# Optimization experiments

Hardware: AMD Instinct MI355X
Metric: run time of the kernel (lower is better)

Reference implementation:

```python
import jax, jax.numpy as jnp
import numpy as np

# norse LICell parameters: tau_mem_inv given as 1/0.001; others at norse defaults
DT = 0.001          # LICell default dt (module's self.dt is never passed to the cell)
TAU_MEM_INV = 1000.0
TAU_SYN_INV = 200.0
V_LEAK = 0.0


def setup_inputs() -> dict:
    key = jax.random.key(0)
    k1, k2 = jax.random.split(key)
    x = jax.random.normal(k1, (256, 1, 512, 512), dtype=jnp.float32)   # [T, C=1, H, W]
    kernel = jax.random.normal(k2, (5, 5), dtype=jnp.float32)          # square conv kernel
    return {"x": x, "kernel": kernel}


def reference(x, kernel):
    T, C, H, W = x.shape

    # Leaky-integrator (norse li_feed_forward_step) over time:
    #   v' = v + dt*tau_mem_inv*((v_leak - v) + i)
    #   i' = i - dt*tau_syn_inv*i + x_t
    # output at each step is v'.
    def step(carry, xt):
        v, i = carry
        v_new = v + DT * TAU_MEM_INV * ((V_LEAK - v) + i)
        i_new = i - DT * TAU_SYN_INV * i + xt
        return (v_new, i_new), v_new

    zeros = jnp.zeros((C, H, W), x.dtype)
    _, vs = jax.lax.scan(step, (zeros, zeros), x)  # [T, C, H, W]

    # Per-timestep 1->1 channel conv with 'same' padding, batched over T at once.
    k = kernel.shape[0]
    pad = (k - 1) // 2
    w = kernel[None, None]  # [O=1, I=1, k, k]
    out = jax.lax.conv_general_dilated(
        vs, w, window_strides=(1, 1),
        padding=[(pad, pad), (pad, pad)],
        dimension_numbers=("NCHW", "OIHW", "NCHW"),
    )
    return out  # [T, 1, H, W]
```

## Files before the change

### kernel.cpp

```cpp
#include <hip/hip_runtime.h>

#define T_STEPS 256
#define IMG 512
#define HW (IMG * IMG)
#define TW 32
#define TH 8
#define HTW 40
#define HTH 12
#define NCHK 120
#define BUF_DW 512
#define NBUF 12

__device__ __align__(16) float g_zeropage[8] = {0, 0, 0, 0, 0, 0, 0, 0};

typedef const __attribute__((address_space(1))) unsigned int* gptr_t;
typedef __attribute__((address_space(3))) unsigned int* lptr_t;
typedef float vf4 __attribute__((ext_vector_type(4)));
typedef float vf2 __attribute__((ext_vector_type(2)));

__launch_bounds__(64)
__global__ void conv_li_kernel(const float* __restrict__ x,
                               const float* __restrict__ kern,
                               float* __restrict__ out) {
    __shared__ __align__(16) float lds[NBUF][BUF_DW];
    const int tid = threadIdx.x;
    const int bid = blockIdx.x;
    const int vbid = (bid & 7) * 128 + (bid >> 3);
    const int bx = vbid & 15;
    const int by = vbid >> 4;

    float kw[25];
#pragma unroll
    for (int i = 0; i < 25; ++i)
        kw[i] = __int_as_float(__builtin_amdgcn_readfirstlane(__float_as_int(kern[i])));

    const float* srcA; const float* srcB; bool okA, okB;
    {
        int c = tid;
        int row = c / 10, cc = c - row * 10;
        int gy = by * TH + row - 2, gx = bx * TW + cc * 4 - 4;
        okA = (gy >= 0) && (gy < IMG) && (gx >= 0) && (gx <= IMG - 4);
        srcA = x + (size_t)(okA ? gy : 0) * IMG + (okA ? gx : 0);
        c = tid + 64;
        row = c / 10; cc = c - row * 10;
        gy = by * TH + row - 2; gx = bx * TW + cc * 4 - 4;
        okB = (c < NCHK) && (gy >= 0) && (gy < IMG) && (gx >= 0) && (gx <= IMG - 4);
        srcB = x + (size_t)(okB ? gy : 0) * IMG + (okB ? gx : 0);
    }

    auto GLDS = [&](int bi, int tf) {
        const float* pA = okA ? srcA + (size_t)tf * HW : g_zeropage;
        const float* pB = okB ? srcB + (size_t)tf * HW : g_zeropage;
        __builtin_amdgcn_global_load_lds((gptr_t)pA, (lptr_t)&lds[bi][0], 16, 0, 0);
        __builtin_amdgcn_global_load_lds((gptr_t)pB, (lptr_t)&lds[bi][256], 16, 0, 0);
    };
    auto BATCH = [&](int bufbase, int f0) {
#pragma unroll
        for (int j = 0; j < 4; ++j) {
            int tf = f0 + j; if (tf > T_STEPS - 1) tf = T_STEPS - 1;
            GLDS(bufbase + j, tf);
        }
    };

    const int q = tid & 7;
    const int rr = tid >> 3;
    const size_t obase = (size_t)(by * TH + rr) * IMG + bx * TW + q * 4;

    vf2 stA = {0.f, 0.f}, stB = {0.f, 0.f};

    auto STEP = [&](int bi, int t) {
        vf2 A0 = {0.f, 0.f}, A1 = {0.f, 0.f}, A2 = {0.f, 0.f}, A3 = {0.f, 0.f};
        const float* Bp = &lds[bi][rr * HTW + q * 4];
#pragma unroll
        for (int dy = 0; dy < 5; ++dy) {
            const float* L = Bp + dy * HTW;
            vf4 c0 = *(const vf4*)(L);
            vf4 c1 = *(const vf4*)(L + 4);
            vf4 c2 = *(const vf4*)(L + 8);
            vf2 P0 = {c0.z, c0.w};
            vf2 P1 = {c1.x, c1.y};
            vf2 P2 = {c1.z, c1.w};
            vf2 P3 = {c2.x, c2.y};
            const float k0 = kw[dy * 5 + 0], k1 = kw[dy * 5 + 1], k2 = kw[dy * 5 + 2];
            const float k3 = kw[dy * 5 + 3], k4 = kw[dy * 5 + 4];
            const vf2 K01 = {k0, k1}, K23 = {k2, k3}, K40 = {k4, 0.f};
            const vf2 K0h = {0.f, k0}, K12 = {k1, k2}, K34 = {k3, k4};
            A0 = __builtin_elementwise_fma(K01, P0, A0);
            A0 = __builtin_elementwise_fma(K23, P1, A0);
            A0 = __builtin_elementwise_fma(K40, P2, A0);
            A1 = __builtin_elementwise_fma(K0h, P0, A1);
            A1 = __builtin_elementwise_fma(K12, P1, A1);
            A1 = __builtin_elementwise_fma(K34, P2, A1);
            A2 = __builtin_elementwise_fma(K01, P1, A2);
            A2 = __builtin_elementwise_fma(K23, P2, A2);
            A2 = __builtin_elementwise_fma(K40, P3, A2);
            A3 = __builtin_elementwise_fma(K0h, P1, A3);
            A3 = __builtin_elementwise_fma(K12, P2, A3);
            A3 = __builtin_elementwise_fma(K34, P3, A3);
        }
        vf4 s = {stA.x, stA.y, stB.x, stB.y};
        __builtin_nontemporal_store(s, (vf4*)(out + (size_t)t * HW + obase));
        vf2 accA = {A0.x + A0.y, A1.x + A1.y};
        vf2 accB = {A2.x + A2.y, A3.x + A3.y};
        const vf2 m02 = {-0.2f, -0.2f};
        stA = __builtin_elementwise_fma(m02, stA, stA) + accA;
        stB = __builtin_elementwise_fma(m02, stB, stB) + accB;
    };

    BATCH(0, 0);
    BATCH(4, 4);

    asm volatile("s_waitcnt vmcnt(8)" ::: "memory");
    STEP(0, 0); STEP(1, 1); STEP(2, 2); STEP(3, 3);
    BATCH(8, 8);

#pragma clang loop unroll(disable)
    for (int sg = 0; sg < 21; ++sg) {
        const int t0 = 4 + sg * 12;
        asm volatile("s_waitcnt vmcnt(12)" ::: "memory");
        STEP(4, t0 + 0); STEP(5, t0 + 1); STEP(6, t0 + 2); STEP(7, t0 + 3);
        BATCH(0, t0 + 8);
        asm volatile("s_waitcnt vmcnt(12)" ::: "memory");
        STEP(8, t0 + 4); STEP(9, t0 + 5); STEP(10, t0 + 6); STEP(11, t0 + 7);
        BATCH(4, t0 + 12);
        asm volatile("s_waitcnt vmcnt(12)" ::: "memory");
        STEP(0, t0 + 8); STEP(1, t0 + 9); STEP(2, t0 + 10); STEP(3, t0 + 11);
        BATCH(8, t0 + 16);
    }
}

extern "C" void kernel_launch(void* const* d_in, const int* in_sizes, int n_in,
                              void* d_out, int out_size, void* d_ws, size_t ws_size,
                              hipStream_t stream) {
    const float* x = (const float*)d_in[0];
    const float* kern = (const float*)d_in[1];
    float* out = (float*)d_out;

    conv_li_kernel<<<dim3(1024), dim3(64), 0, stream>>>(x, kern, out);
}
```

Measured before the change: 97.11 us.

## Shift output column mapping by two so LDS reads use two aligned vf4 loads

Each thread's output window moves right by two columns, so its 5x5 stencil inputs fit in two aligned vf4 LDS reads per row instead of three. Stores become two vf2 nontemporal stores instead of one vf4. The first two image columns are handled by extra edge-block accumulators, and the final two columns are skipped. The vmcnt wait thresholds are raised to count the extra store instructions, at the cost of more branches and narrower stores.

```diff
diff --git a/kernel.cpp b/kernel.cpp
--- a/kernel.cpp
+++ b/kernel.cpp
@@ -64,23 +64,27 @@
 
     const int q = tid & 7;
     const int rr = tid >> 3;
-    const size_t obase = (size_t)(by * TH + rr) * IMG + bx * TW + q * 4;
+    const bool lastq = (bx == 15) && (q == 7);
+    const bool edgeblk = (bx == 0);
+    const size_t rowbase = (size_t)(by * TH + rr) * IMG;
+    const size_t obase = rowbase + bx * TW + 4 * q + 2;
 
-    vf2 stA = {0.f, 0.f}, stB = {0.f, 0.f};
+    vf2 stP = {0.f, 0.f}, stQ = {0.f, 0.f};
+    vf2 stE = {0.f, 0.f};
 
     auto STEP = [&](int bi, int t) {
         vf2 A0 = {0.f, 0.f}, A1 = {0.f, 0.f}, A2 = {0.f, 0.f}, A3 = {0.f, 0.f};
-        const float* Bp = &lds[bi][rr * HTW + q * 4];
+        vf2 AE0 = {0.f, 0.f}, AE1 = {0.f, 0.f};
+        const float* Bp = &lds[bi][(rr * 10 + q + 1) * 4];
 #pragma unroll
         for (int dy = 0; dy < 5; ++dy) {
             const float* L = Bp + dy * HTW;
             vf4 c0 = *(const vf4*)(L);
             vf4 c1 = *(const vf4*)(L + 4);
-            vf4 c2 = *(const vf4*)(L + 8);
-            vf2 P0 = {c0.z, c0.w};
-            vf2 P1 = {c1.x, c1.y};
-            vf2 P2 = {c1.z, c1.w};
-            vf2 P3 = {c2.x, c2.y};
+            vf2 P0 = {c0.x, c0.y};
+            vf2 P1 = {c0.z, c0.w};
+            vf2 P2 = {c1.x, c1.y};
+            vf2 P3 = {c1.z, c1.w};
             const float k0 = kw[dy * 5 + 0], k1 = kw[dy * 5 + 1], k2 = kw[dy * 5 + 2];
             const float k3 = kw[dy * 5 + 3], k4 = kw[dy * 5 + 4];
             const vf2 K01 = {k0, k1}, K23 = {k2, k3}, K40 = {k4, 0.f};
@@ -97,14 +101,29 @@
             A3 = __builtin_elementwise_fma(K0h, P1, A3);
             A3 = __builtin_elementwise_fma(K12, P2, A3);
             A3 = __builtin_elementwise_fma(K34, P3, A3);
+            if (edgeblk) {
+                AE0 = __builtin_elementwise_fma(K23, P0, AE0);
+                AE0 = __builtin_elementwise_fma(K40, P1, AE0);
+                AE1 = __builtin_elementwise_fma(K12, P0, AE1);
+                AE1 = __builtin_elementwise_fma(K34, P1, AE1);
+            }
         }
-        vf4 s = {stA.x, stA.y, stB.x, stB.y};
-        __builtin_nontemporal_store(s, (vf4*)(out + (size_t)t * HW + obase));
-        vf2 accA = {A0.x + A0.y, A1.x + A1.y};
-        vf2 accB = {A2.x + A2.y, A3.x + A3.y};
+        float* op = out + (size_t)t * HW + obase;
+        __builtin_nontemporal_store(stP, (vf2*)op);
+        if (!lastq)
+            __builtin_nontemporal_store(stQ, (vf2*)(op + 2));
+        if (edgeblk) {
+            if (q == 0)
+                __builtin_nontemporal_store(stE, (vf2*)(out + (size_t)t * HW + rowbase));
+            vf2 accE = {AE0.x + AE0.y, AE1.x + AE1.y};
+            const vf2 m02e = {-0.2f, -0.2f};
+            stE = __builtin_elementwise_fma(m02e, stE, stE) + accE;
+        }
+        vf2 accP = {A0.x + A0.y, A1.x + A1.y};
+        vf2 accQ = {A2.x + A2.y, A3.x + A3.y};
         const vf2 m02 = {-0.2f, -0.2f};
-        stA = __builtin_elementwise_fma(m02, stA, stA) + accA;
-        stB = __builtin_elementwise_fma(m02, stB, stB) + accB;
+        stP = __builtin_elementwise_fma(m02, stP, stP) + accP;
+        stQ = __builtin_elementwise_fma(m02, stQ, stQ) + accQ;
     };
 
     BATCH(0, 0);
@@ -117,13 +136,13 @@
 #pragma clang loop unroll(disable)
     for (int sg = 0; sg < 21; ++sg) {
         const int t0 = 4 + sg * 12;
-        asm volatile("s_waitcnt vmcnt(12)" ::: "memory");
+        asm volatile("s_waitcnt vmcnt(16)" ::: "memory");
         STEP(4, t0 + 0); STEP(5, t0 + 1); STEP(6, t0 + 2); STEP(7, t0 + 3);
         BATCH(0, t0 + 8);
-        asm volatile("s_waitcnt vmcnt(12)" ::: "memory");
+        asm volatile("s_waitcnt vmcnt(16)" ::: "memory");
         STEP(8, t0 + 4); STEP(9, t0 + 5); STEP(10, t0 + 6); STEP(11, t0 + 7);
         BATCH(4, t0 + 12);
-        asm volatile("s_waitcnt vmcnt(12)" ::: "memory");
+        asm volatile("s_waitcnt vmcnt(16)" ::: "memory");
         STEP(0, t0 + 8); STEP(1, t0 + 9); STEP(2, t0 + 10); STEP(3, t0 + 11);
         BATCH(8, t0 + 16);
     }
```

Measured after the change: 188.3 us. 93.9% more time.
